# Optimization experiments

Hardware: AMD Instinct MI355X
Metric: run time of the kernel (lower is better)

The kernel has to match this reference:

```python
import jax, jax.numpy as jnp
import numpy as np

N = 100000   # num_nodes
E = 600000   # num_edges (before self loops)
H = 128      # hidden_size
R = 16       # lora_rank
SCALING = 32.0 / 16  # lora_alpha / lora_rank
LN_EPS = 1e-5


def setup_inputs() -> dict:
    key = jax.random.key(0)
    ks = jax.random.split(key, 12)
    s = 0.02
    return {
        "hidden_states": jax.random.normal(ks[0], (N, H), dtype=jnp.float32),
        "edge_index": jax.random.randint(ks[1], (2, E), 0, N, dtype=jnp.int64),
        # message_transform (LoRALinear): base W/b + lora A/B
        "msg_W": jax.random.normal(ks[2], (H, H), dtype=jnp.float32) * s,
        "msg_b": jax.random.normal(ks[3], (H,), dtype=jnp.float32) * s,
        "msg_A": jax.random.normal(ks[4], (R, H), dtype=jnp.float32) * s,
        "msg_B": jax.random.normal(ks[5], (H, R), dtype=jnp.float32) * s,
        # gate_transform (LoRALinear)
        "gate_W": jax.random.normal(ks[6], (H, H), dtype=jnp.float32) * s,
        "gate_b": jax.random.normal(ks[7], (H,), dtype=jnp.float32) * s,
        "gate_A": jax.random.normal(ks[8], (R, H), dtype=jnp.float32) * s,
        "gate_B": jax.random.normal(ks[9], (H, R), dtype=jnp.float32) * s,
        # LayerNorm params
        "ln_gamma": jnp.ones((H,), dtype=jnp.float32),
        "ln_beta": jnp.zeros((H,), dtype=jnp.float32),
    }


def _lora_linear(x, W, b, A, B):
    # base_layer(x) + scaling * lora_B(lora_A(x)); dropout is identity at eval
    return x @ W.T + b + SCALING * ((x @ A.T) @ B.T)


def _message_passing(x, edge_index):
    n = x.shape[0]
    loops = jnp.arange(n, dtype=edge_index.dtype)
    row = jnp.concatenate([edge_index[0], loops])  # sources j
    col = jnp.concatenate([edge_index[1], loops])  # targets i
    # symmetric-ish norm: deg from targets (PyG degree(col))
    deg = jax.ops.segment_sum(jnp.ones_like(col, dtype=x.dtype), col, num_segments=n)
    dinv = jnp.where(deg > 0, deg ** -0.5, 0.0)
    norm = dinv[row] * dinv[col]                   # [E+N]
    msgs = norm[:, None] * x[row]                  # edge-gathered messages
    summed = jax.ops.segment_sum(msgs, col, num_segments=n)
    # aggr='mean': divide by per-target edge count (== deg, includes self loop)
    return summed / jnp.maximum(deg, 1.0)[:, None]


def reference(hidden_states, edge_index, msg_W, msg_b, msg_A, msg_B,
              gate_W, gate_b, gate_A, gate_B, ln_gamma, ln_beta):
    message_out = _message_passing(hidden_states, edge_index)
    message_transformed = _lora_linear(message_out, msg_W, msg_b, msg_A, msg_B)
    gate = jax.nn.sigmoid(_lora_linear(hidden_states, gate_W, gate_b, gate_A, gate_B))
    x = hidden_states + gate * message_transformed
    mu = jnp.mean(x, axis=-1, keepdims=True)
    var = jnp.mean(jnp.square(x - mu), axis=-1, keepdims=True)
    return (x - mu) / jnp.sqrt(var + LN_EPS) * ln_gamma + ln_beta
```

## Files before the change

kernel.cpp:

```cpp
#include <hip/hip_runtime.h>
#include <math.h>

#define H 128
#define RANK 16
#define SCALING 2.0f
#define LN_EPS 1e-5f
#define PAD 32

typedef short bf16x8 __attribute__((ext_vector_type(8)));
typedef float f32x4 __attribute__((ext_vector_type(4)));

__device__ __forceinline__ unsigned short f2bf(float f) {
    unsigned int u = __float_as_uint(f);
    u += 0x7fffu + ((u >> 16) & 1u);
    return (unsigned short)(u >> 16);
}
__device__ __forceinline__ unsigned int pk2(float a, float b) {
    return (unsigned int)f2bf(a) | ((unsigned int)f2bf(b) << 16);
}
__device__ __forceinline__ float bflo(unsigned int u) {
    return __uint_as_float(u << 16);
}
__device__ __forceinline__ float bfhi(unsigned int u) {
    return __uint_as_float(u & 0xffff0000u);
}

__global__ __launch_bounds__(256) void k_init(
    const int* __restrict__ ei, int E,
    int* __restrict__ deg, int* __restrict__ adj,
    const float4* __restrict__ x4, int total16, unsigned int* __restrict__ xb,
    uint4* __restrict__ xq4,
    const float* __restrict__ msg_W, const float* __restrict__ msg_A,
    const float* __restrict__ msg_B,
    const float* __restrict__ gate_W, const float* __restrict__ gate_A,
    const float* __restrict__ gate_B,
    unsigned short* __restrict__ Wmz, unsigned short* __restrict__ Wgz,
    float* __restrict__ rsq_tbl,
    int BA, int BB) {
    int b = blockIdx.x;
    int t = threadIdx.x;
    if (b < BA) {
        int q = b * 256 + t;
        int e0 = q * 8;
        if ((E & 7) == 0) {
            if (e0 < E) {
                const int4* colv = (const int4*)(ei + E);
                const int4* srcv = (const int4*)ei;
                int4 c0 = colv[q * 2], c1 = colv[q * 2 + 1];
                int4 s0 = srcv[q * 2], s1 = srcv[q * 2 + 1];
                int cc[8] = {c0.x, c0.y, c0.z, c0.w, c1.x, c1.y, c1.z, c1.w};
                int ss[8] = {s0.x, s0.y, s0.z, s0.w, s1.x, s1.y, s1.z, s1.w};
                int pos[8];
                #pragma unroll
                for (int j = 0; j < 8; ++j) pos[j] = atomicAdd(&deg[cc[j]], 1);
                #pragma unroll
                for (int j = 0; j < 8; ++j)
                    if (pos[j] < PAD) adj[cc[j] * PAD + pos[j]] = ss[j];
            }
        } else {
            #pragma unroll
            for (int j = 0; j < 8; ++j) {
                int e = e0 + j;
                if (e < E) {
                    int c = ei[E + e];
                    int pos = atomicAdd(&deg[c], 1);
                    if (pos < PAD) adj[c * PAD + pos] = ei[e];
                }
            }
        }
    } else if (b < BA + BB) {
        int idx = (b - BA) * 256 + t;
        if (idx < total16) {
            float4 a = x4[idx * 4 + 0];
            float4 bq = x4[idx * 4 + 1];
            float4 cq = x4[idx * 4 + 2];
            float4 dq = x4[idx * 4 + 3];
            uint4 o0, o1;
            o0.x = pk2(a.x, a.y);   o0.y = pk2(a.z, a.w);
            o0.z = pk2(bq.x, bq.y); o0.w = pk2(bq.z, bq.w);
            o1.x = pk2(cq.x, cq.y); o1.y = pk2(cq.z, cq.w);
            o1.z = pk2(dq.x, dq.y); o1.w = pk2(dq.z, dq.w);
            uint4* xb4 = (uint4*)xb;
            xb4[idx * 2 + 0] = o0;
            xb4[idx * 2 + 1] = o1;
            int q0 = __builtin_amdgcn_cvt_pk_fp8_f32(a.x, a.y, 0, false);
            q0 = __builtin_amdgcn_cvt_pk_fp8_f32(a.z, a.w, q0, true);
            int q1 = __builtin_amdgcn_cvt_pk_fp8_f32(bq.x, bq.y, 0, false);
            q1 = __builtin_amdgcn_cvt_pk_fp8_f32(bq.z, bq.w, q1, true);
            int q2 = __builtin_amdgcn_cvt_pk_fp8_f32(cq.x, cq.y, 0, false);
            q2 = __builtin_amdgcn_cvt_pk_fp8_f32(cq.z, cq.w, q2, true);
            int q3 = __builtin_amdgcn_cvt_pk_fp8_f32(dq.x, dq.y, 0, false);
            q3 = __builtin_amdgcn_cvt_pk_fp8_f32(dq.z, dq.w, q3, true);
            uint4 oq;
            oq.x = (unsigned int)q0; oq.y = (unsigned int)q1;
            oq.z = (unsigned int)q2; oq.w = (unsigned int)q3;
            xq4[idx] = oq;
        }
    } else if (b < BA + BB + 128) {
        int bb = b - BA - BB;
        int which = bb >> 6;
        int idx = (bb & 63) * 256 + t;
        const float* W = which ? gate_W : msg_W;
        const float* A = which ? gate_A : msg_A;
        const float* Bm = which ? gate_B : msg_B;
        unsigned short* Wz = which ? Wgz : Wmz;
        int h = idx & (H - 1);
        int k = idx >> 7;
        float s = 0.f;
        #pragma unroll
        for (int r = 0; r < RANK; ++r) s = fmaf(A[r * H + k], Bm[h * RANK + r], s);
        float v = W[h * H + k] + SCALING * s;
        int kt = k >> 5, kk = k & 31, qd = kk >> 3, j = kk & 7;
        int nt = h >> 4, nl = h & 15;
        int lane = qd * 16 + nl;
        Wz[(((kt * 8 + nt) * 64 + lane) * 8) + j] = f2bf(v);
    } else {
        if (t < 64) rsq_tbl[t] = rsqrtf((float)(t + 1));
    }
}

__global__ __launch_bounds__(256) void k_gather(
    const unsigned int* __restrict__ xb, const unsigned short* __restrict__ xq16,
    const int* __restrict__ adj,
    const int* __restrict__ deg, const float* __restrict__ rsq_tbl,
    int N, unsigned int* __restrict__ msgb) {
    int wave = (blockIdx.x * 256 + threadIdx.x) >> 6;
    int lane = threadIdx.x & 63;
    if (wave >= N) return;
    int i = __builtin_amdgcn_readfirstlane(wave);
    int dg = __builtin_amdgcn_readfirstlane(deg[i]);
    int dcap = dg < 63 ? dg : 63;
    float di = rsq_tbl[dcap];
    float dif = (float)(dg + 1);
    unsigned int su = xb[(size_t)i * 64 + lane];
    float ax[8], ay[8];
    ax[0] = bflo(su) * di; ay[0] = bfhi(su) * di;
    #pragma unroll
    for (int j = 1; j < 8; ++j) { ax[j] = 0.f; ay[j] = 0.f; }
    int cnt = dg < PAD ? dg : PAD;
    int s0 = i * PAD, s1 = s0 + cnt;
    int last = s1 - 1;
    for (int e = s0; e < s1; e += 8) {
        int is[8]; float ws[8]; unsigned short us[8];
        #pragma unroll
        for (int j = 0; j < 8; ++j) {
            int ee = e + j;
            is[j] = __builtin_amdgcn_readfirstlane(adj[ee < s1 ? ee : last]);
        }
        #pragma unroll
        for (int j = 0; j < 8; ++j) {
            int dj = deg[is[j]];
            dj = dj < 63 ? dj : 63;
            float w = rsq_tbl[dj];
            ws[j] = (e + j < s1) ? w : 0.f;
        }
        #pragma unroll
        for (int j = 0; j < 8; ++j) us[j] = xq16[(size_t)is[j] * 64 + lane];
        #pragma unroll
        for (int j = 0; j < 8; ++j) {
            float lo = __builtin_amdgcn_cvt_f32_fp8((int)us[j], 0);
            float hi = __builtin_amdgcn_cvt_f32_fp8((int)us[j], 1);
            ax[j] = fmaf(ws[j], lo, ax[j]);
            ay[j] = fmaf(ws[j], hi, ay[j]);
        }
    }
    float sc = di / dif;
    float rx = (((ax[0] + ax[1]) + (ax[2] + ax[3])) + ((ax[4] + ax[5]) + (ax[6] + ax[7]))) * sc;
    float ry = (((ay[0] + ay[1]) + (ay[2] + ay[3])) + ((ay[4] + ay[5]) + (ay[6] + ay[7]))) * sc;
    msgb[(size_t)i * 64 + lane] = (unsigned int)f2bf(rx) | ((unsigned int)f2bf(ry) << 16);
}

__global__ __launch_bounds__(256) void k_fused(
    const unsigned int* __restrict__ xb, const unsigned int* __restrict__ msgb,
    const unsigned short* __restrict__ Wmz, const unsigned short* __restrict__ Wgz,
    const float* __restrict__ msg_b, const float* __restrict__ gate_b,
    const float* __restrict__ gamma, const float* __restrict__ beta,
    float* __restrict__ out, int N) {
    __shared__ unsigned int hLds[64 * 64];
    int t = threadIdx.x;
    int wid = t >> 6, lane = t & 63;
    int m0 = (blockIdx.x * 4 + wid) * 16;
    if (m0 >= N) return;

    char* rowbase = (char*)(hLds + wid * 16 * 64);

    #pragma unroll
    for (int r16 = 0; r16 < 16; ++r16) {
        int rr = m0 + r16; if (rr >= N) rr = N - 1;
        unsigned int v = xb[(size_t)rr * 64 + lane];
        int wbyte = ((r16 * 64 + lane) << 2) ^ ((r16 & 7) << 4);
        *(unsigned int*)(rowbase + wbyte) = v;
    }

    int quad = lane >> 4;
    int nl = lane & 15;

    int arow = m0 + nl; if (arow >= N) arow = N - 1;
    const bf16x8* mb8 = (const bf16x8*)msgb + (size_t)arow * 16;

    f32x4 accg[8], accm[8];
    #pragma unroll
    for (int nt = 0; nt < 8; ++nt) {
        accg[nt] = (f32x4)(0.f);
        accm[nt] = (f32x4)(0.f);
    }

    #pragma unroll
    for (int kt = 0; kt < 4; ++kt) {
        int abyte = (nl * 256 + kt * 64 + quad * 16) ^ ((nl & 7) << 4);
        bf16x8 ah = *(const bf16x8*)(rowbase + abyte);
        bf16x8 am = mb8[kt * 4 + quad];
        const bf16x8* bg8 = (const bf16x8*)(Wgz + (size_t)kt * 4096);
        const bf16x8* bm8 = (const bf16x8*)(Wmz + (size_t)kt * 4096);
        #pragma unroll
        for (int nt = 0; nt < 8; ++nt) {
            bf16x8 bg = bg8[nt * 64 + lane];
            bf16x8 bm = bm8[nt * 64 + lane];
            accg[nt] = __builtin_amdgcn_mfma_f32_16x16x32_bf16(ah, bg, accg[nt], 0, 0, 0);
            accm[nt] = __builtin_amdgcn_mfma_f32_16x16x32_bf16(am, bm, accm[nt], 0, 0, 0);
        }
    }

    float gb[8], mb[8], gm[8], bt[8];
    #pragma unroll
    for (int nt = 0; nt < 8; ++nt) {
        int col = nt * 16 + nl;
        gb[nt] = gate_b[col]; mb[nt] = msg_b[col];
        gm[nt] = gamma[col];  bt[nt] = beta[col];
    }

    #pragma unroll
    for (int r = 0; r < 4; ++r) {
        int row = quad * 4 + r;
        int node = m0 + row;
        float xr[8]; float s = 0.f, ss = 0.f;
        #pragma unroll
        for (int nt = 0; nt < 8; ++nt) {
            int col = nt * 16 + nl;
            int hbyte = (row * 256 + col * 2) ^ ((row & 7) << 4);
            unsigned short hu = *(const unsigned short*)(rowbase + hbyte);
            float hv = __uint_as_float((unsigned int)hu << 16);
            float g = 1.f / (1.f + __expf(-(accg[nt][r] + gb[nt])));
            float m = accm[nt][r] + mb[nt];
            float v = fmaf(g, m, hv);
            xr[nt] = v; s += v; ss = fmaf(v, v, ss);
        }
        #pragma unroll
        for (int msk = 1; msk < 16; msk <<= 1) {
            s += __shfl_xor(s, msk);
            ss += __shfl_xor(ss, msk);
        }
        float mu = s * (1.f / 128.f);
        float var = ss * (1.f / 128.f) - mu * mu;
        float rstd = rsqrtf(var + LN_EPS);
        if (node < N) {
            float* orow = out + (size_t)node * H;
            #pragma unroll
            for (int nt = 0; nt < 8; ++nt)
                orow[nt * 16 + nl] = (xr[nt] - mu) * rstd * gm[nt] + bt[nt];
        }
    }
}

extern "C" void kernel_launch(void* const* d_in, const int* in_sizes, int n_in,
                              void* d_out, int out_size, void* d_ws, size_t ws_size,
                              hipStream_t stream) {
    const float* hidden = (const float*)d_in[0];
    const int*   ei     = (const int*)d_in[1];
    const float* msg_W  = (const float*)d_in[2];
    const float* msg_b  = (const float*)d_in[3];
    const float* msg_A  = (const float*)d_in[4];
    const float* msg_B  = (const float*)d_in[5];
    const float* gate_W = (const float*)d_in[6];
    const float* gate_b = (const float*)d_in[7];
    const float* gate_A = (const float*)d_in[8];
    const float* gate_B = (const float*)d_in[9];
    const float* gamma  = (const float*)d_in[10];
    const float* beta   = (const float*)d_in[11];
    float* out = (float*)d_out;

    int N = in_sizes[0] / H;
    int E = in_sizes[1] / 2;

    char* p = (char*)d_ws;
    unsigned short* Wmz = (unsigned short*)p;  p += (size_t)H * H * sizeof(unsigned short);
    unsigned short* Wgz = (unsigned short*)p;  p += (size_t)H * H * sizeof(unsigned short);
    unsigned int* xb   = (unsigned int*)p;     p += (size_t)N * 64 * sizeof(unsigned int);
    unsigned int* msgb = (unsigned int*)p;     p += (size_t)N * 64 * sizeof(unsigned int);
    int* deg = (int*)p;                        p += (size_t)N * sizeof(int);
    float* rsq_tbl = (float*)p;                p += 64 * sizeof(float);

    int* adj = (int*)d_out;
    unsigned char* xq = (unsigned char*)d_out + (16u << 20);

    hipMemsetAsync(deg, 0, (size_t)N * sizeof(int), stream);

    int BA = (E + 2047) / 2048;
    int total16 = (N * H) >> 4;
    int BB = (total16 + 255) / 256;

    k_init<<<BA + BB + 128 + 1, 256, 0, stream>>>(
        ei, E, deg, adj, (const float4*)hidden, total16, xb, (uint4*)xq,
        msg_W, msg_A, msg_B, gate_W, gate_A, gate_B, Wmz, Wgz, rsq_tbl, BA, BB);

    k_gather<<<((size_t)N * 64 + 255) / 256, 256, 0, stream>>>(
        xb, (const unsigned short*)xq, adj, deg, rsq_tbl, N, msgb);

    int waves = (N + 15) / 16;
    k_fused<<<(waves + 3) / 4, 256, 0, stream>>>(
        xb, msgb, Wmz, Wgz, msg_b, gate_b, gamma, beta, out, N);
}
```

Baseline: 236.9 us.

## Merge init and gather kernels into one persistent kernel with a grid barrier

Fuses the preprocessing kernel (degree counting, adjacency build, bf16/fp8 conversion, LoRA weight folding) and the neighbour-gather kernel into one persistent kernel of 2048 blocks. The two phases are separated by a software grid barrier built on an atomic counter, and the work is spread with grid-stride loops. This removes one kernel launch and the idle gap between the two kernels. The barrier is only safe if all 2048 blocks are resident at once, which relies on the occupancy hint of 8 blocks per CU; otherwise it can deadlock. The barrier counter is cleared by extending the existing memset.

```diff
diff --git a/kernel.cpp b/kernel.cpp
--- a/kernel.cpp
+++ b/kernel.cpp
@@ -6,6 +6,7 @@
 #define SCALING 2.0f
 #define LN_EPS 1e-5f
 #define PAD 32
+#define NBLK 2048
 
 typedef short bf16x8 __attribute__((ext_vector_type(8)));
 typedef float f32x4 __attribute__((ext_vector_type(4)));
@@ -25,8 +26,20 @@
     return __uint_as_float(u & 0xffff0000u);
 }
 
-__global__ __launch_bounds__(256) void k_init(
-    const int* __restrict__ ei, int E,
+__device__ __forceinline__ void gridbar(int* cnt, int nblk) {
+    __syncthreads();
+    if (threadIdx.x == 0) {
+        __threadfence();
+        __hip_atomic_fetch_add(cnt, 1, __ATOMIC_RELEASE, __HIP_MEMORY_SCOPE_AGENT);
+        while (__hip_atomic_load(cnt, __ATOMIC_ACQUIRE, __HIP_MEMORY_SCOPE_AGENT) < nblk)
+            __builtin_amdgcn_s_sleep(1);
+        __threadfence();
+    }
+    __syncthreads();
+}
+
+__global__ __launch_bounds__(256, 8) void k_front(
+    const int* __restrict__ ei, int E, int N,
     int* __restrict__ deg, int* __restrict__ adj,
     const float4* __restrict__ x4, int total16, unsigned int* __restrict__ xb,
     uint4* __restrict__ xq4,
@@ -35,29 +48,29 @@
     const float* __restrict__ gate_W, const float* __restrict__ gate_A,
     const float* __restrict__ gate_B,
     unsigned short* __restrict__ Wmz, unsigned short* __restrict__ Wgz,
-    float* __restrict__ rsq_tbl,
-    int BA, int BB) {
-    int b = blockIdx.x;
+    float* __restrict__ rsq_tbl, int* __restrict__ bar,
+    unsigned int* __restrict__ msgb) {
     int t = threadIdx.x;
-    if (b < BA) {
-        int q = b * 256 + t;
-        int e0 = q * 8;
+    int gtid = blockIdx.x * 256 + t;
+    int nth = gridDim.x * 256;
+
+    int nq = (E + 7) / 8;
+    for (int q = gtid; q < nq; q += nth) {
         if ((E & 7) == 0) {
-            if (e0 < E) {
-                const int4* colv = (const int4*)(ei + E);
-                const int4* srcv = (const int4*)ei;
-                int4 c0 = colv[q * 2], c1 = colv[q * 2 + 1];
-                int4 s0 = srcv[q * 2], s1 = srcv[q * 2 + 1];
-                int cc[8] = {c0.x, c0.y, c0.z, c0.w, c1.x, c1.y, c1.z, c1.w};
-                int ss[8] = {s0.x, s0.y, s0.z, s0.w, s1.x, s1.y, s1.z, s1.w};
-                int pos[8];
-                #pragma unroll
-                for (int j = 0; j < 8; ++j) pos[j] = atomicAdd(&deg[cc[j]], 1);
-                #pragma unroll
-                for (int j = 0; j < 8; ++j)
-                    if (pos[j] < PAD) adj[cc[j] * PAD + pos[j]] = ss[j];
-            }
+            const int4* colv = (const int4*)(ei + E);
+            const int4* srcv = (const int4*)ei;
+            int4 c0 = colv[q * 2], c1 = colv[q * 2 + 1];
+            int4 s0 = srcv[q * 2], s1 = srcv[q * 2 + 1];
+            int cc[8] = {c0.x, c0.y, c0.z, c0.w, c1.x, c1.y, c1.z, c1.w};
+            int ss[8] = {s0.x, s0.y, s0.z, s0.w, s1.x, s1.y, s1.z, s1.w};
+            int pos[8];
+            #pragma unroll
+            for (int j = 0; j < 8; ++j) pos[j] = atomicAdd(&deg[cc[j]], 1);
+            #pragma unroll
+            for (int j = 0; j < 8; ++j)
+                if (pos[j] < PAD) adj[cc[j] * PAD + pos[j]] = ss[j];
         } else {
+            int e0 = q * 8;
             #pragma unroll
             for (int j = 0; j < 8; ++j) {
                 int e = e0 + j;
@@ -68,44 +81,44 @@
                 }
             }
         }
-    } else if (b < BA + BB) {
-        int idx = (b - BA) * 256 + t;
-        if (idx < total16) {
-            float4 a = x4[idx * 4 + 0];
-            float4 bq = x4[idx * 4 + 1];
-            float4 cq = x4[idx * 4 + 2];
-            float4 dq = x4[idx * 4 + 3];
-            uint4 o0, o1;
-            o0.x = pk2(a.x, a.y);   o0.y = pk2(a.z, a.w);
-            o0.z = pk2(bq.x, bq.y); o0.w = pk2(bq.z, bq.w);
-            o1.x = pk2(cq.x, cq.y); o1.y = pk2(cq.z, cq.w);
-            o1.z = pk2(dq.x, dq.y); o1.w = pk2(dq.z, dq.w);
-            uint4* xb4 = (uint4*)xb;
-            xb4[idx * 2 + 0] = o0;
-            xb4[idx * 2 + 1] = o1;
-            int q0 = __builtin_amdgcn_cvt_pk_fp8_f32(a.x, a.y, 0, false);
-            q0 = __builtin_amdgcn_cvt_pk_fp8_f32(a.z, a.w, q0, true);
-            int q1 = __builtin_amdgcn_cvt_pk_fp8_f32(bq.x, bq.y, 0, false);
-            q1 = __builtin_amdgcn_cvt_pk_fp8_f32(bq.z, bq.w, q1, true);
-            int q2 = __builtin_amdgcn_cvt_pk_fp8_f32(cq.x, cq.y, 0, false);
-            q2 = __builtin_amdgcn_cvt_pk_fp8_f32(cq.z, cq.w, q2, true);
-            int q3 = __builtin_amdgcn_cvt_pk_fp8_f32(dq.x, dq.y, 0, false);
-            q3 = __builtin_amdgcn_cvt_pk_fp8_f32(dq.z, dq.w, q3, true);
-            uint4 oq;
-            oq.x = (unsigned int)q0; oq.y = (unsigned int)q1;
-            oq.z = (unsigned int)q2; oq.w = (unsigned int)q3;
-            xq4[idx] = oq;
-        }
-    } else if (b < BA + BB + 128) {
-        int bb = b - BA - BB;
-        int which = bb >> 6;
-        int idx = (bb & 63) * 256 + t;
+    }
+
+    for (int idx = gtid; idx < total16; idx += nth) {
+        float4 a = x4[idx * 4 + 0];
+        float4 bq = x4[idx * 4 + 1];
+        float4 cq = x4[idx * 4 + 2];
+        float4 dq = x4[idx * 4 + 3];
+        uint4 o0, o1;
+        o0.x = pk2(a.x, a.y);   o0.y = pk2(a.z, a.w);
+        o0.z = pk2(bq.x, bq.y); o0.w = pk2(bq.z, bq.w);
+        o1.x = pk2(cq.x, cq.y); o1.y = pk2(cq.z, cq.w);
+        o1.z = pk2(dq.x, dq.y); o1.w = pk2(dq.z, dq.w);
+        uint4* xb4 = (uint4*)xb;
+        xb4[idx * 2 + 0] = o0;
+        xb4[idx * 2 + 1] = o1;
+        int q0 = __builtin_amdgcn_cvt_pk_fp8_f32(a.x, a.y, 0, false);
+        q0 = __builtin_amdgcn_cvt_pk_fp8_f32(a.z, a.w, q0, true);
+        int q1 = __builtin_amdgcn_cvt_pk_fp8_f32(bq.x, bq.y, 0, false);
+        q1 = __builtin_amdgcn_cvt_pk_fp8_f32(bq.z, bq.w, q1, true);
+        int q2 = __builtin_amdgcn_cvt_pk_fp8_f32(cq.x, cq.y, 0, false);
+        q2 = __builtin_amdgcn_cvt_pk_fp8_f32(cq.z, cq.w, q2, true);
+        int q3 = __builtin_amdgcn_cvt_pk_fp8_f32(dq.x, dq.y, 0, false);
+        q3 = __builtin_amdgcn_cvt_pk_fp8_f32(dq.z, dq.w, q3, true);
+        uint4 oq;
+        oq.x = (unsigned int)q0; oq.y = (unsigned int)q1;
+        oq.z = (unsigned int)q2; oq.w = (unsigned int)q3;
+        xq4[idx] = oq;
+    }
+
+    for (int idx = gtid; idx < 2 * H * H; idx += nth) {
+        int which = idx >> 14;
+        int li = idx & (H * H - 1);
         const float* W = which ? gate_W : msg_W;
         const float* A = which ? gate_A : msg_A;
         const float* Bm = which ? gate_B : msg_B;
         unsigned short* Wz = which ? Wgz : Wmz;
-        int h = idx & (H - 1);
-        int k = idx >> 7;
+        int h = li & (H - 1);
+        int k = li >> 7;
         float s = 0.f;
         #pragma unroll
         for (int r = 0; r < RANK; ++r) s = fmaf(A[r * H + k], Bm[h * RANK + r], s);
@@ -114,60 +127,57 @@
         int nt = h >> 4, nl = h & 15;
         int lane = qd * 16 + nl;
         Wz[(((kt * 8 + nt) * 64 + lane) * 8) + j] = f2bf(v);
-    } else {
-        if (t < 64) rsq_tbl[t] = rsqrtf((float)(t + 1));
-    }
-}
-
-__global__ __launch_bounds__(256) void k_gather(
-    const unsigned int* __restrict__ xb, const unsigned short* __restrict__ xq16,
-    const int* __restrict__ adj,
-    const int* __restrict__ deg, const float* __restrict__ rsq_tbl,
-    int N, unsigned int* __restrict__ msgb) {
-    int wave = (blockIdx.x * 256 + threadIdx.x) >> 6;
-    int lane = threadIdx.x & 63;
-    if (wave >= N) return;
-    int i = __builtin_amdgcn_readfirstlane(wave);
-    int dg = __builtin_amdgcn_readfirstlane(deg[i]);
-    int dcap = dg < 63 ? dg : 63;
-    float di = rsq_tbl[dcap];
-    float dif = (float)(dg + 1);
-    unsigned int su = xb[(size_t)i * 64 + lane];
-    float ax[8], ay[8];
-    ax[0] = bflo(su) * di; ay[0] = bfhi(su) * di;
-    #pragma unroll
-    for (int j = 1; j < 8; ++j) { ax[j] = 0.f; ay[j] = 0.f; }
-    int cnt = dg < PAD ? dg : PAD;
-    int s0 = i * PAD, s1 = s0 + cnt;
-    int last = s1 - 1;
-    for (int e = s0; e < s1; e += 8) {
-        int is[8]; float ws[8]; unsigned short us[8];
-        #pragma unroll
-        for (int j = 0; j < 8; ++j) {
-            int ee = e + j;
-            is[j] = __builtin_amdgcn_readfirstlane(adj[ee < s1 ? ee : last]);
-        }
-        #pragma unroll
-        for (int j = 0; j < 8; ++j) {
-            int dj = deg[is[j]];
-            dj = dj < 63 ? dj : 63;
-            float w = rsq_tbl[dj];
-            ws[j] = (e + j < s1) ? w : 0.f;
-        }
-        #pragma unroll
-        for (int j = 0; j < 8; ++j) us[j] = xq16[(size_t)is[j] * 64 + lane];
-        #pragma unroll
-        for (int j = 0; j < 8; ++j) {
-            float lo = __builtin_amdgcn_cvt_f32_fp8((int)us[j], 0);
-            float hi = __builtin_amdgcn_cvt_f32_fp8((int)us[j], 1);
-            ax[j] = fmaf(ws[j], lo, ax[j]);
-            ay[j] = fmaf(ws[j], hi, ay[j]);
-        }
-    }
-    float sc = di / dif;
-    float rx = (((ax[0] + ax[1]) + (ax[2] + ax[3])) + ((ax[4] + ax[5]) + (ax[6] + ax[7]))) * sc;
-    float ry = (((ay[0] + ay[1]) + (ay[2] + ay[3])) + ((ay[4] + ay[5]) + (ay[6] + ay[7]))) * sc;
-    msgb[(size_t)i * 64 + lane] = (unsigned int)f2bf(rx) | ((unsigned int)f2bf(ry) << 16);
+    }
+
+    if (gtid < 64) rsq_tbl[gtid] = rsqrtf((float)(gtid + 1));
+
+    gridbar(bar, gridDim.x);
+
+    int waveId = gtid >> 6, lane = t & 63, nwaves = nth >> 6;
+    const unsigned short* xq16 = (const unsigned short*)xq4;
+    for (int node = waveId; node < N; node += nwaves) {
+        int i = __builtin_amdgcn_readfirstlane(node);
+        int dg = __builtin_amdgcn_readfirstlane(deg[i]);
+        int dcap = dg < 63 ? dg : 63;
+        float di = rsq_tbl[dcap];
+        float dif = (float)(dg + 1);
+        unsigned int su = xb[(size_t)i * 64 + lane];
+        float ax[8], ay[8];
+        ax[0] = bflo(su) * di; ay[0] = bfhi(su) * di;
+        #pragma unroll
+        for (int j = 1; j < 8; ++j) { ax[j] = 0.f; ay[j] = 0.f; }
+        int cnt = dg < PAD ? dg : PAD;
+        int s0 = i * PAD, s1 = s0 + cnt;
+        int last = s1 - 1;
+        for (int e = s0; e < s1; e += 8) {
+            int is[8]; float ws[8]; unsigned short us[8];
+            #pragma unroll
+            for (int j = 0; j < 8; ++j) {
+                int ee = e + j;
+                is[j] = __builtin_amdgcn_readfirstlane(adj[ee < s1 ? ee : last]);
+            }
+            #pragma unroll
+            for (int j = 0; j < 8; ++j) {
+                int dj = deg[is[j]];
+                dj = dj < 63 ? dj : 63;
+                float w = rsq_tbl[dj];
+                ws[j] = (e + j < s1) ? w : 0.f;
+            }
+            #pragma unroll
+            for (int j = 0; j < 8; ++j) us[j] = xq16[(size_t)is[j] * 64 + lane];
+            #pragma unroll
+            for (int j = 0; j < 8; ++j) {
+                float lo = __builtin_amdgcn_cvt_f32_fp8((int)us[j], 0);
+                float hi = __builtin_amdgcn_cvt_f32_fp8((int)us[j], 1);
+                ax[j] = fmaf(ws[j], lo, ax[j]);
+                ay[j] = fmaf(ws[j], hi, ay[j]);
+            }
+        }
+        float sc = di / dif;
+        float rx = (((ax[0] + ax[1]) + (ax[2] + ax[3])) + ((ax[4] + ax[5]) + (ax[6] + ax[7]))) * sc;
+        float ry = (((ay[0] + ay[1]) + (ay[2] + ay[3])) + ((ay[4] + ay[5]) + (ay[6] + ay[7]))) * sc;
+        msgb[(size_t)node * 64 + lane] = (unsigned int)f2bf(rx) | ((unsigned int)f2bf(ry) << 16);
+    }
 }
 
 __global__ __launch_bounds__(256) void k_fused(
@@ -265,16 +275,9 @@
 extern "C" void kernel_launch(void* const* d_in, const int* in_sizes, int n_in,
                               void* d_out, int out_size, void* d_ws, size_t ws_size,
                               hipStream_t stream) {
-    const float* hidden = (const float*)d_in[0];
     const int*   ei     = (const int*)d_in[1];
-    const float* msg_W  = (const float*)d_in[2];
     const float* msg_b  = (const float*)d_in[3];
-    const float* msg_A  = (const float*)d_in[4];
-    const float* msg_B  = (const float*)d_in[5];
-    const float* gate_W = (const float*)d_in[6];
     const float* gate_b = (const float*)d_in[7];
-    const float* gate_A = (const float*)d_in[8];
-    const float* gate_B = (const float*)d_in[9];
     const float* gamma  = (const float*)d_in[10];
     const float* beta   = (const float*)d_in[11];
     float* out = (float*)d_out;
@@ -288,23 +291,21 @@
     unsigned int* xb   = (unsigned int*)p;     p += (size_t)N * 64 * sizeof(unsigned int);
     unsigned int* msgb = (unsigned int*)p;     p += (size_t)N * 64 * sizeof(unsigned int);
     int* deg = (int*)p;                        p += (size_t)N * sizeof(int);
+    int* bar = (int*)p;                        p += 2 * sizeof(int);
     float* rsq_tbl = (float*)p;                p += 64 * sizeof(float);
 
     int* adj = (int*)d_out;
     unsigned char* xq = (unsigned char*)d_out + (16u << 20);
 
-    hipMemsetAsync(deg, 0, (size_t)N * sizeof(int), stream);
-
-    int BA = (E + 2047) / 2048;
+    hipMemsetAsync(deg, 0, ((size_t)N + 2) * sizeof(int), stream);
+
     int total16 = (N * H) >> 4;
-    int BB = (total16 + 255) / 256;
-
-    k_init<<<BA + BB + 128 + 1, 256, 0, stream>>>(
-        ei, E, deg, adj, (const float4*)hidden, total16, xb, (uint4*)xq,
-        msg_W, msg_A, msg_B, gate_W, gate_A, gate_B, Wmz, Wgz, rsq_tbl, BA, BB);
-
-    k_gather<<<((size_t)N * 64 + 255) / 256, 256, 0, stream>>>(
-        xb, (const unsigned short*)xq, adj, deg, rsq_tbl, N, msgb);
+
+    k_front<<<NBLK, 256, 0, stream>>>(
+        ei, E, N, deg, adj, (const float4*)d_in[0], total16, xb, (uint4*)xq,
+        (const float*)d_in[2], (const float*)d_in[4], (const float*)d_in[5],
+        (const float*)d_in[6], (const float*)d_in[8], (const float*)d_in[9],
+        Wmz, Wgz, rsq_tbl, bar, msgb);
 
     int waves = (N + 15) / 16;
     k_fused<<<(waves + 3) / 4, 256, 0, stream>>>(
```

Result: slower. 687.7 us (+190.2%).
